# Optimization experiments

Measured on AMD Instinct MI355X. Metric: run time of the kernel, lower is better.

The kernel has to match this reference:

```python
import jax, jax.numpy as jnp
import numpy as np

BN_EPS = 1e-5
NEG_SLOPE = 0.2

def _avgpool2(x):
    B, C, H, W = x.shape
    return x.reshape(B, C, H // 2, 2, W // 2, 2).mean(axis=(3, 5))

def _conv1x1(x, w, b):
    # x: [B,C,H,W], w: [O,C], b: [O]
    return jnp.einsum('bchw,oc->bohw', x, w) + b[None, :, None, None]

def _bilinear_resize(x, out_h, out_w):
    # PyTorch F.interpolate(mode='bilinear', align_corners=False) semantics
    B, C, h, w = x.shape
    ys = jnp.maximum((jnp.arange(out_h, dtype=jnp.float32) + 0.5) * (h / out_h) - 0.5, 0.0)
    xs = jnp.maximum((jnp.arange(out_w, dtype=jnp.float32) + 0.5) * (w / out_w) - 0.5, 0.0)
    y0 = jnp.floor(ys).astype(jnp.int32); x0 = jnp.floor(xs).astype(jnp.int32)
    wy = (ys - y0.astype(jnp.float32)).astype(x.dtype)
    wx = (xs - x0.astype(jnp.float32)).astype(x.dtype)
    y1 = jnp.minimum(y0 + 1, h - 1); x1 = jnp.minimum(x0 + 1, w - 1)
    rows = x[:, :, y0, :] * (1.0 - wy)[None, None, :, None] + x[:, :, y1, :] * wy[None, None, :, None]
    out = rows[:, :, :, x0] * (1.0 - wx)[None, None, None, :] + rows[:, :, :, x1] * wx[None, None, None, :]
    return out

def setup_inputs() -> dict:
    key = jax.random.key(0)
    ks = jax.random.split(key, 16)
    B, Cin, Hid, Cout, H, W = 8, 64, 64, 64, 128, 128
    s = 0.05
    return {
        'rgb': jax.random.normal(ks[0], (B, Cin, H, W), dtype=jnp.float32),
        'freq': jax.random.normal(ks[1], (B, Cin, H, W), dtype=jnp.float32),
        'w_q': jax.random.normal(ks[2], (Hid, Cin), dtype=jnp.float32) * s,
        'b_q': jax.random.normal(ks[3], (Hid,), dtype=jnp.float32) * s,
        'w_k': jax.random.normal(ks[4], (Hid, Cin), dtype=jnp.float32) * s,
        'b_k': jax.random.normal(ks[5], (Hid,), dtype=jnp.float32) * s,
        'w_v': jax.random.normal(ks[6], (Hid, Cin), dtype=jnp.float32) * s,
        'b_v': jax.random.normal(ks[7], (Hid,), dtype=jnp.float32) * s,
        'w_o': jax.random.normal(ks[8], (Cout, Hid), dtype=jnp.float32) * s,
        'b_o': jax.random.normal(ks[9], (Cout,), dtype=jnp.float32) * s,
        'bn_gamma': jnp.ones((Cout,), dtype=jnp.float32),
        'bn_beta': jnp.zeros((Cout,), dtype=jnp.float32),
        'bn_mean': jax.random.normal(ks[10], (Cout,), dtype=jnp.float32) * s,
        'bn_var': jax.random.uniform(ks[11], (Cout,), dtype=jnp.float32, minval=0.5, maxval=1.5),
    }

def reference(rgb, freq, w_q, b_q, w_k, b_k, w_v, b_v, w_o, b_o, bn_gamma, bn_beta, bn_mean, bn_var):
    B, C, H, W = rgb.shape
    rgb_ds = _avgpool2(rgb)
    freq_ds = _avgpool2(freq)
    hd, wd = rgb_ds.shape[2], rgb_ds.shape[3]
    hid = w_q.shape[0]
    scale = hid ** (-0.5)
    # 1x1 conv QKV projections, flatten spatial dims to tokens N = hd*wd
    q = _conv1x1(rgb_ds, w_q, b_q).reshape(B, hid, hd * wd)   # [B,hid,N]
    k = _conv1x1(freq_ds, w_k, b_k).reshape(B, hid, hd * wd)  # [B,hid,N]
    v = _conv1x1(freq_ds, w_v, b_v).reshape(B, hid, hd * wd)  # [B,hid,N]
    attn = jax.nn.softmax(jnp.einsum('bcn,bcm->bnm', q, k) * scale, axis=-1)  # [B,N,N]
    z = jnp.einsum('bnm,bcm->bcn', attn, v).reshape(B, hid, hd, wd)
    z = _bilinear_resize(z, H, W)
    y = _conv1x1(z, w_o, b_o)
    # inference-mode BatchNorm fused as affine
    inv = bn_gamma / jnp.sqrt(bn_var + BN_EPS)
    y = (y - bn_mean[None, :, None, None]) * inv[None, :, None, None] + bn_beta[None, :, None, None]
    y = jnp.where(y >= 0, y, NEG_SLOPE * y)  # LeakyReLU(0.2)
    return rgb + y
```

## Files before the change

kernel.cpp:

```cpp
#include <hip/hip_runtime.h>
#include <hip/hip_bf16.h>

typedef unsigned short u16;
typedef unsigned int   u32;
typedef __attribute__((ext_vector_type(8))) short bf16x8;
typedef __attribute__((ext_vector_type(4))) float f32x4;

__device__ __forceinline__ u16 f2bf(float f) {
  u32 u = __float_as_uint(f);
  u32 r = u + 0x7fffu + ((u >> 16) & 1u);
  return (u16)(r >> 16);
}
__device__ __forceinline__ float bflo(u32 u) { return __uint_as_float(u << 16); }
__device__ __forceinline__ float bfhi(u32 u) { return __uint_as_float(u & 0xffff0000u); }
__device__ __forceinline__ u32 packhi(float a, float b) {
  return __builtin_amdgcn_perm(__float_as_uint(b), __float_as_uint(a), 0x07060302u);
}

__global__ __launch_bounds__(256, 4) void k_qkv(
    const float* __restrict__ rgb, const float* __restrict__ freq,
    const float* __restrict__ wq, const float* __restrict__ bq,
    const float* __restrict__ wk, const float* __restrict__ bk,
    const float* __restrict__ wv, const float* __restrict__ bv,
    u16* __restrict__ Qo, u16* __restrict__ Ko, u16* __restrict__ Vo)
{
  __shared__ __align__(16) u16 sm[3 * 4608];
  u16* X  = sm;
  u16* W0 = sm + 4608;
  u16* W1 = sm + 9216;

  const int t    = threadIdx.x;
  const int side = blockIdx.x & 1;
  const int seg  = blockIdx.x >> 1;
  const int idx0 = seg * 64;
  const int bb   = idx0 >> 12;
  const int n0   = idx0 & 4095;
  const int h    = n0 >> 6;
  const float* src = side ? freq : rgb;

  const size_t sbase = (size_t)bb * 64 * 16384 + (size_t)(2 * h) * 128;
  {
    const int tokp = t & 31;
    const int grp  = t >> 5;
    const float* p0 = src + sbase + 4 * tokp + (size_t)(grp * 8) * 16384;
    u32 pk0[4], pk1[4];
#pragma unroll
    for (int c = 0; c < 8; c += 2) {
      const float* pa = p0 + (size_t)c * 16384;
      float4 a0 = *(const float4*)pa;
      float4 a1 = *(const float4*)(pa + 128);
      float t0a = 0.25f * ((a0.x + a0.y) + (a1.x + a1.y));
      float t1a = 0.25f * ((a0.z + a0.w) + (a1.z + a1.w));
      const float* pb = pa + 16384;
      float4 c0 = *(const float4*)pb;
      float4 c1 = *(const float4*)(pb + 128);
      float t0b = 0.25f * ((c0.x + c0.y) + (c1.x + c1.y));
      float t1b = 0.25f * ((c0.z + c0.w) + (c1.z + c1.w));
      pk0[c >> 1] = (u32)f2bf(t0a) | ((u32)f2bf(t0b) << 16);
      pk1[c >> 1] = (u32)f2bf(t1a) | ((u32)f2bf(t1b) << 16);
    }
    uint4 qv0; qv0.x = pk0[0]; qv0.y = pk0[1]; qv0.z = pk0[2]; qv0.w = pk0[3];
    uint4 qv1; qv1.x = pk1[0]; qv1.y = pk1[1]; qv1.z = pk1[2]; qv1.w = pk1[3];
    *(uint4*)&X[(2 * tokp) * 72 + grp * 8] = qv0;
    *(uint4*)&X[(2 * tokp + 1) * 72 + grp * 8] = qv1;
  }
  {
    const int o = t >> 2, c0 = (t & 3) << 4;
    const float4* p4 = (const float4*)((side ? wk : wq) + o * 64 + c0);
    float4 f0 = p4[0], f1 = p4[1], f2 = p4[2], f3 = p4[3];
    uint4 qa, qb;
    qa.x = (u32)f2bf(f0.x) | ((u32)f2bf(f0.y) << 16);
    qa.y = (u32)f2bf(f0.z) | ((u32)f2bf(f0.w) << 16);
    qa.z = (u32)f2bf(f1.x) | ((u32)f2bf(f1.y) << 16);
    qa.w = (u32)f2bf(f1.z) | ((u32)f2bf(f1.w) << 16);
    qb.x = (u32)f2bf(f2.x) | ((u32)f2bf(f2.y) << 16);
    qb.y = (u32)f2bf(f2.z) | ((u32)f2bf(f2.w) << 16);
    qb.z = (u32)f2bf(f3.x) | ((u32)f2bf(f3.y) << 16);
    qb.w = (u32)f2bf(f3.z) | ((u32)f2bf(f3.w) << 16);
    *(uint4*)&W0[o * 72 + c0] = qa;
    *(uint4*)&W0[o * 72 + c0 + 8] = qb;
    if (side) {
      const float4* v4 = (const float4*)(wv + o * 64 + c0);
      float4 g0 = v4[0], g1 = v4[1], g2 = v4[2], g3 = v4[3];
      qa.x = (u32)f2bf(g0.x) | ((u32)f2bf(g0.y) << 16);
      qa.y = (u32)f2bf(g0.z) | ((u32)f2bf(g0.w) << 16);
      qa.z = (u32)f2bf(g1.x) | ((u32)f2bf(g1.y) << 16);
      qa.w = (u32)f2bf(g1.z) | ((u32)f2bf(g1.w) << 16);
      qb.x = (u32)f2bf(g2.x) | ((u32)f2bf(g2.y) << 16);
      qb.y = (u32)f2bf(g2.z) | ((u32)f2bf(g2.w) << 16);
      qb.z = (u32)f2bf(g3.x) | ((u32)f2bf(g3.y) << 16);
      qb.w = (u32)f2bf(g3.z) | ((u32)f2bf(g3.w) << 16);
      *(uint4*)&W1[o * 72 + c0] = qa;
      *(uint4*)&W1[o * 72 + c0 + 8] = qb;
    }
  }
  __syncthreads();

  const int lane = t & 63, w = t >> 6;
  const int l15 = lane & 15, qd = lane >> 4;
  const int tb = w * 16;

  bf16x8 af0 = *(const bf16x8*)&X[(tb + l15) * 72 + qd * 8];
  bf16x8 af1 = *(const bf16x8*)&X[(tb + l15) * 72 + 32 + qd * 8];

  f32x4 acc[4];
#pragma unroll
  for (int nt = 0; nt < 4; ++nt) {
    bf16x8 b0 = *(const bf16x8*)&W0[(nt * 16 + l15) * 72 + qd * 8];
    bf16x8 b1 = *(const bf16x8*)&W0[(nt * 16 + l15) * 72 + 32 + qd * 8];
    f32x4 a = {0.f, 0.f, 0.f, 0.f};
    a = __builtin_amdgcn_mfma_f32_16x16x32_bf16(af0, b0, a, 0, 0, 0);
    a = __builtin_amdgcn_mfma_f32_16x16x32_bf16(af1, b1, a, 0, 0, 0);
    acc[nt] = a;
  }
  {
    const float* bias0 = side ? bk : bq;
    const float sc = side ? 1.f : 0.18033688f;
    u16* dst0 = side ? Ko : Qo;
#pragma unroll
    for (int nt = 0; nt < 4; ++nt) {
      float bia = bias0[nt * 16 + l15];
#pragma unroll
      for (int e = 0; e < 4; ++e) {
        int tok = idx0 + tb + qd * 4 + e;
        dst0[(size_t)tok * 64 + nt * 16 + l15] = f2bf((acc[nt][e] + bia) * sc);
      }
    }
  }

  if (side) {
    f32x4 accv[4];
#pragma unroll
    for (int ct = 0; ct < 4; ++ct) {
      bf16x8 a0 = *(const bf16x8*)&W1[(ct * 16 + l15) * 72 + qd * 8];
      bf16x8 a1 = *(const bf16x8*)&W1[(ct * 16 + l15) * 72 + 32 + qd * 8];
      f32x4 a = {0.f, 0.f, 0.f, 0.f};
      a = __builtin_amdgcn_mfma_f32_16x16x32_bf16(a0, af0, a, 0, 0, 0);
      a = __builtin_amdgcn_mfma_f32_16x16x32_bf16(a1, af1, a, 0, 0, 0);
      accv[ct] = a;
    }
#pragma unroll
    for (int ct = 0; ct < 4; ++ct) {
#pragma unroll
      for (int e = 0; e < 4; ++e) {
        int c = ct * 16 + qd * 4 + e;
        float v = accv[ct][e] + bv[c];
        Vo[((size_t)(bb * 64 + c)) * 4096 + n0 + tb + l15] = f2bf(v);
      }
    }
  }
}

__global__ __launch_bounds__(256, 2) void k_attn(
    const u16* __restrict__ Qg, const u16* __restrict__ Kg,
    const u16* __restrict__ Vg,
    const float* __restrict__ wo, const float* __restrict__ bo,
    const float* __restrict__ gam, const float* __restrict__ bet,
    const float* __restrict__ mean, const float* __restrict__ var,
    u16* __restrict__ Ya)
{
  __shared__ __align__(16) u16 Pb[4 * 4608];
  __shared__ __align__(16) u16 Wl[4608];
  __shared__ __align__(16) u16 Zc[4608];
  __shared__ float lb[256];
  __shared__ float Afs[64], Bfs[64];

  const int b  = blockIdx.x;
  const int q0 = blockIdx.y * 64;
  const int t  = threadIdx.x;
  const int lane = t & 63, w = t >> 6;
  const int l15 = lane & 15, qd = lane >> 4;
  u16* P = Pb + w * 4608;

  {
    const int o = t >> 2, c0 = (t & 3) << 4;
    const float4* p4 = (const float4*)(wo + o * 64 + c0);
    float4 f0 = p4[0], f1 = p4[1], f2 = p4[2], f3 = p4[3];
    uint4 qa, qb;
    qa.x = (u32)f2bf(f0.x) | ((u32)f2bf(f0.y) << 16);
    qa.y = (u32)f2bf(f0.z) | ((u32)f2bf(f0.w) << 16);
    qa.z = (u32)f2bf(f1.x) | ((u32)f2bf(f1.y) << 16);
    qa.w = (u32)f2bf(f1.z) | ((u32)f2bf(f1.w) << 16);
    qb.x = (u32)f2bf(f2.x) | ((u32)f2bf(f2.y) << 16);
    qb.y = (u32)f2bf(f2.z) | ((u32)f2bf(f2.w) << 16);
    qb.z = (u32)f2bf(f3.x) | ((u32)f2bf(f3.y) << 16);
    qb.w = (u32)f2bf(f3.z) | ((u32)f2bf(f3.w) << 16);
    *(uint4*)&Wl[o * 72 + c0] = qa;
    *(uint4*)&Wl[o * 72 + c0 + 8] = qb;
    if (t < 64) {
      float A = gam[t] * __frsqrt_rn(var[t] + 1e-5f);
      Afs[t] = A;
      Bfs[t] = (bo[t] - mean[t]) * A + bet[t];
    }
  }

  bf16x8 qf[4][2];
#pragma unroll
  for (int qt = 0; qt < 4; ++qt) {
    const u16* p = Qg + ((size_t)(b * 4096 + q0 + qt * 16 + l15)) * 64 + qd * 8;
    qf[qt][0] = *(const bf16x8*)p;
    qf[qt][1] = *(const bf16x8*)(p + 32);
  }

  f32x4 zacc[4][4];
#pragma unroll
  for (int i = 0; i < 4; ++i)
#pragma unroll
    for (int j = 0; j < 4; ++j) {
      f32x4 z = {0.f, 0.f, 0.f, 0.f};
      zacc[i][j] = z;
    }
  float lacc[4] = {0.f, 0.f, 0.f, 0.f};

  for (int tile = 0; tile < 16; ++tile) {
    const int n0 = w * 1024 + tile * 64;

    bf16x8 kf[4][2], vf[4][2];
#pragma unroll
    for (int mt = 0; mt < 4; ++mt) {
      const u16* p = Kg + ((size_t)(b * 4096 + n0 + mt * 16 + l15)) * 64 + qd * 8;
      kf[mt][0] = *(const bf16x8*)p;
      kf[mt][1] = *(const bf16x8*)(p + 32);
    }
#pragma unroll
    for (int ct = 0; ct < 4; ++ct) {
      const u16* p = Vg + ((size_t)(b * 64 + ct * 16 + l15)) * 4096 + n0 + qd * 8;
      vf[ct][0] = *(const bf16x8*)p;
      vf[ct][1] = *(const bf16x8*)(p + 32);
    }

#pragma unroll
    for (int qt = 0; qt < 4; ++qt) {
#pragma unroll
      for (int mt = 0; mt < 4; ++mt) {
        f32x4 a = {0.f, 0.f, 0.f, 0.f};
        __builtin_amdgcn_s_setprio(1);
        a = __builtin_amdgcn_mfma_f32_16x16x32_bf16(kf[mt][0], qf[qt][0], a, 0, 0, 0);
        a = __builtin_amdgcn_mfma_f32_16x16x32_bf16(kf[mt][1], qf[qt][1], a, 0, 0, 0);
        __builtin_amdgcn_s_setprio(0);
        float p0 = __builtin_amdgcn_exp2f(a[0]);
        float p1 = __builtin_amdgcn_exp2f(a[1]);
        float p2 = __builtin_amdgcn_exp2f(a[2]);
        float p3 = __builtin_amdgcn_exp2f(a[3]);
        lacc[qt] += (p0 + p1) + (p2 + p3);
        uint2 pw;
        pw.x = packhi(p0, p1);
        pw.y = packhi(p2, p3);
        *(uint2*)&P[(qt * 16 + l15) * 72 + mt * 16 + qd * 4] = pw;
      }
    }
#pragma unroll
    for (int qt = 0; qt < 4; ++qt) {
      bf16x8 pf0 = *(const bf16x8*)&P[(qt * 16 + l15) * 72 + qd * 8];
      bf16x8 pf1 = *(const bf16x8*)&P[(qt * 16 + l15) * 72 + 32 + qd * 8];
      __builtin_amdgcn_s_setprio(1);
#pragma unroll
      for (int ct = 0; ct < 4; ++ct) {
        zacc[ct][qt] = __builtin_amdgcn_mfma_f32_16x16x32_bf16(vf[ct][0], pf0, zacc[ct][qt], 0, 0, 0);
        zacc[ct][qt] = __builtin_amdgcn_mfma_f32_16x16x32_bf16(vf[ct][1], pf1, zacc[ct][qt], 0, 0, 0);
      }
      __builtin_amdgcn_s_setprio(0);
    }
  }

#pragma unroll
  for (int qt = 0; qt < 4; ++qt) {
    float l = lacc[qt];
    l += __shfl_xor(l, 16);
    l += __shfl_xor(l, 32);
    lb[w * 64 + qt * 16 + l15] = l;
  }
#pragma unroll
  for (int qt = 0; qt < 4; ++qt)
#pragma unroll
    for (int ct = 0; ct < 4; ++ct) {
      uint2 pw;
      pw.x = packhi(zacc[ct][qt][0], zacc[ct][qt][1]);
      pw.y = packhi(zacc[ct][qt][2], zacc[ct][qt][3]);
      *(uint2*)&P[(qt * 16 + l15) * 72 + ct * 16 + qd * 4] = pw;
    }
  __syncthreads();

  {
    const u32* Pu = (const u32*)Pb;
    u32* Zu = (u32*)Zc;
#pragma unroll
    for (int i = 0; i < 8; ++i) {
      int cell = i * 256 + t;
      int q = cell >> 5, cu = cell & 31;
      float s0 = 0.f, s1 = 0.f;
#pragma unroll
      for (int ww = 0; ww < 4; ++ww) {
        u32 v = Pu[ww * 2304 + q * 36 + cu];
        s0 += bflo(v);
        s1 += bfhi(v);
      }
      float inv = 1.f / (lb[q] + lb[64 + q] + lb[128 + q] + lb[192 + q]);
      Zu[q * 36 + cu] = packhi(s0 * inv, s1 * inv);
    }
  }
  __syncthreads();

  {
    u16* Ys = Pb;
    bf16x8 af0 = *(const bf16x8*)&Zc[(w * 16 + l15) * 72 + qd * 8];
    bf16x8 af1 = *(const bf16x8*)&Zc[(w * 16 + l15) * 72 + 32 + qd * 8];
#pragma unroll
    for (int nt = 0; nt < 4; ++nt) {
      bf16x8 b0 = *(const bf16x8*)&Wl[(nt * 16 + l15) * 72 + qd * 8];
      bf16x8 b1 = *(const bf16x8*)&Wl[(nt * 16 + l15) * 72 + 32 + qd * 8];
      f32x4 y = {0.f, 0.f, 0.f, 0.f};
      y = __builtin_amdgcn_mfma_f32_16x16x32_bf16(b0, af0, y, 0, 0, 0);
      y = __builtin_amdgcn_mfma_f32_16x16x32_bf16(b1, af1, y, 0, 0, 0);
#pragma unroll
      for (int e = 0; e < 4; ++e) {
        const int o = nt * 16 + qd * 4 + e;
        float v = y[e] * Afs[o] + Bfs[o];
        Ys[o * 72 + w * 16 + l15] = (u16)(__float_as_uint(v) >> 16);
      }
    }
  }
  __syncthreads();
  {
    const int o = t >> 2, c4 = (t & 3) << 4;
    uint4 y0 = *(const uint4*)&Pb[o * 72 + c4];
    uint4 y1 = *(const uint4*)&Pb[o * 72 + c4 + 8];
    u16* d = Ya + ((size_t)(b * 64 + o)) * 4096 + q0;
    *(uint4*)&d[c4] = y0;
    *(uint4*)&d[c4 + 8] = y1;
  }
}

__global__ __launch_bounds__(256, 8) void k_out(
    const u16* __restrict__ Ya, const float* __restrict__ rgb,
    float* __restrict__ out)
{
  const int tid = blockIdx.x * 256 + threadIdx.x;
  const int g = tid & 31;
  const int i = (tid >> 5) & 127;
  const int o = (tid >> 12) & 63;
  const int b = tid >> 18;

  float ys = fmaxf(0.5f * (float)i - 0.25f, 0.f);
  int   y0 = (int)ys;
  float wy = ys - (float)y0;
  int   y1 = min(y0 + 1, 63);

  const u32* Yw = (const u32*)(Ya + ((size_t)(b * 64 + o)) * 4096);
  const int base0 = y0 * 32, base1 = y1 * 32;
  const int gm = (g == 0) ? 0 : g - 1;
  const int gp = (g == 31) ? 31 : g + 1;

  u32 tm = Yw[base0 + gm], t0 = Yw[base0 + g], tp = Yw[base0 + gp];
  u32 bm = Yw[base1 + gm], b0w = Yw[base1 + g], bp = Yw[base1 + gp];

  const float iw = 1.f - wy;
  float r_m1 = iw * bfhi(tm) + wy * bfhi(bm);
  float r_0  = iw * bflo(t0) + wy * bflo(b0w);
  float r_1  = iw * bfhi(t0) + wy * bfhi(b0w);
  float r_2  = iw * bflo(tp) + wy * bflo(bp);

  float v0 = (g == 0)  ? r_0 : 0.25f * r_m1 + 0.75f * r_0;
  float v1 = 0.75f * r_0 + 0.25f * r_1;
  float v2 = 0.25f * r_0 + 0.75f * r_1;
  float v3 = (g == 31) ? r_1 : 0.75f * r_1 + 0.25f * r_2;

  v0 = (v0 >= 0.f) ? v0 : 0.2f * v0;
  v1 = (v1 >= 0.f) ? v1 : 0.2f * v1;
  v2 = (v2 >= 0.f) ? v2 : 0.2f * v2;
  v3 = (v3 >= 0.f) ? v3 : 0.2f * v3;

  const size_t pix = ((size_t)((b * 64 + o) * 128 + i)) * 128 + g * 4;
  float4 rv = *(const float4*)(rgb + pix);
  float4 ov;
  ov.x = rv.x + v0;
  ov.y = rv.y + v1;
  ov.z = rv.z + v2;
  ov.w = rv.w + v3;
  *(float4*)(out + pix) = ov;
}

extern "C" void kernel_launch(void* const* d_in, const int* in_sizes, int n_in,
                              void* d_out, int out_size, void* d_ws, size_t ws_size,
                              hipStream_t stream) {
  (void)in_sizes; (void)n_in; (void)out_size; (void)ws_size;
  const float* rgb  = (const float*)d_in[0];
  const float* freq = (const float*)d_in[1];
  const float* wq   = (const float*)d_in[2];
  const float* bq   = (const float*)d_in[3];
  const float* wk   = (const float*)d_in[4];
  const float* bk   = (const float*)d_in[5];
  const float* wv   = (const float*)d_in[6];
  const float* bv   = (const float*)d_in[7];
  const float* wo   = (const float*)d_in[8];
  const float* bo   = (const float*)d_in[9];
  const float* gam  = (const float*)d_in[10];
  const float* bet  = (const float*)d_in[11];
  const float* mean = (const float*)d_in[12];
  const float* var  = (const float*)d_in[13];

  char* ws = (char*)d_ws;
  u16* Qw = (u16*)(ws);
  u16* Kw = (u16*)(ws + 4194304);
  u16* Vw = (u16*)(ws + 8388608);
  u16* Yw = (u16*)(ws + 12582912);

  k_qkv<<<dim3(1024), dim3(256), 0, stream>>>(rgb, freq, wq, bq, wk, bk, wv, bv,
                                              Qw, Kw, Vw);
  k_attn<<<dim3(8, 64), dim3(256), 0, stream>>>(Qw, Kw, Vw, wo, bo, gam, bet,
                                                mean, var, Yw);
  k_out<<<dim3(8192), dim3(256), 0, stream>>>(Yw, rgb, (float*)d_out);
}
```

Measured before the change: 200.7 us.

## Halve attention query tile per block and split keys across two wave pairs

The attention kernel now handles 32 queries per block instead of 64, launching twice as many blocks. Waves are arranged as 2 query halves × 2 key splits instead of 4 key splits, with per-wave register and shared-memory footprints shrunk and launch bounds raised for higher occupancy. This targets low occupancy and poor latency hiding from large per-wave accumulators, at the cost of reloading each K/V tile for half as many queries, which doubles K/V global traffic.

Result: slower. 361.0 us (+79.9%).

```diff
diff --git a/kernel.cpp b/kernel.cpp
--- a/kernel.cpp
+++ b/kernel.cpp
@@ -151,7 +151,7 @@
   }
 }
 
-__global__ __launch_bounds__(256, 2) void k_attn(
+__global__ __launch_bounds__(256, 4) void k_attn(
     const u16* __restrict__ Qg, const u16* __restrict__ Kg,
     const u16* __restrict__ Vg,
     const float* __restrict__ wo, const float* __restrict__ bo,
@@ -159,18 +159,19 @@
     const float* __restrict__ mean, const float* __restrict__ var,
     u16* __restrict__ Ya)
 {
-  __shared__ __align__(16) u16 Pb[4 * 4608];
+  __shared__ __align__(16) u16 Pb[4 * 1152];
   __shared__ __align__(16) u16 Wl[4608];
-  __shared__ __align__(16) u16 Zc[4608];
-  __shared__ float lb[256];
+  __shared__ __align__(16) u16 Zc[2304];
+  __shared__ float lb[64];
   __shared__ float Afs[64], Bfs[64];
 
   const int b  = blockIdx.x;
-  const int q0 = blockIdx.y * 64;
+  const int q0 = blockIdx.y * 32;
   const int t  = threadIdx.x;
   const int lane = t & 63, w = t >> 6;
+  const int qh = w & 1, ks = w >> 1;
   const int l15 = lane & 15, qd = lane >> 4;
-  u16* P = Pb + w * 4608;
+  u16* P = Pb + w * 1152;
 
   {
     const int o = t >> 2, c0 = (t & 3) << 4;
@@ -194,34 +195,51 @@
     }
   }
 
-  bf16x8 qf[4][2];
-#pragma unroll
-  for (int qt = 0; qt < 4; ++qt) {
-    const u16* p = Qg + ((size_t)(b * 4096 + q0 + qt * 16 + l15)) * 64 + qd * 8;
-    qf[qt][0] = *(const bf16x8*)p;
-    qf[qt][1] = *(const bf16x8*)(p + 32);
-  }
-
-  f32x4 zacc[4][4];
-#pragma unroll
-  for (int i = 0; i < 4; ++i)
-#pragma unroll
-    for (int j = 0; j < 4; ++j) {
-      f32x4 z = {0.f, 0.f, 0.f, 0.f};
-      zacc[i][j] = z;
-    }
-  float lacc[4] = {0.f, 0.f, 0.f, 0.f};
-
-  for (int tile = 0; tile < 16; ++tile) {
-    const int n0 = w * 1024 + tile * 64;
-
-    bf16x8 kf[4][2], vf[4][2];
+  bf16x8 qf0, qf1;
+  {
+    const u16* p = Qg + ((size_t)(b * 4096 + q0 + qh * 16 + l15)) * 64 + qd * 8;
+    qf0 = *(const bf16x8*)p;
+    qf1 = *(const bf16x8*)(p + 32);
+  }
+
+  f32x4 zacc[4];
+#pragma unroll
+  for (int i = 0; i < 4; ++i) {
+    f32x4 z = {0.f, 0.f, 0.f, 0.f};
+    zacc[i] = z;
+  }
+  float lacc = 0.f;
+
+  for (int tile = 0; tile < 32; ++tile) {
+    const int n0 = ks * 2048 + tile * 64;
+
+    bf16x8 kf[4][2];
 #pragma unroll
     for (int mt = 0; mt < 4; ++mt) {
       const u16* p = Kg + ((size_t)(b * 4096 + n0 + mt * 16 + l15)) * 64 + qd * 8;
       kf[mt][0] = *(const bf16x8*)p;
       kf[mt][1] = *(const bf16x8*)(p + 32);
     }
+
+#pragma unroll
+    for (int mt = 0; mt < 4; ++mt) {
+      f32x4 a = {0.f, 0.f, 0.f, 0.f};
+      __builtin_amdgcn_s_setprio(1);
+      a = __builtin_amdgcn_mfma_f32_16x16x32_bf16(kf[mt][0], qf0, a, 0, 0, 0);
+      a = __builtin_amdgcn_mfma_f32_16x16x32_bf16(kf[mt][1], qf1, a, 0, 0, 0);
+      __builtin_amdgcn_s_setprio(0);
+      float p0 = __builtin_amdgcn_exp2f(a[0]);
+      float p1 = __builtin_amdgcn_exp2f(a[1]);
+      float p2 = __builtin_amdgcn_exp2f(a[2]);
+      float p3 = __builtin_amdgcn_exp2f(a[3]);
+      lacc += (p0 + p1) + (p2 + p3);
+      uint2 pw;
+      pw.x = packhi(p0, p1);
+      pw.y = packhi(p2, p3);
+      *(uint2*)&P[l15 * 72 + mt * 16 + qd * 4] = pw;
+    }
+
+    bf16x8 vf[4][2];
 #pragma unroll
     for (int ct = 0; ct < 4; ++ct) {
       const u16* p = Vg + ((size_t)(b * 64 + ct * 16 + l15)) * 4096 + n0 + qd * 8;
@@ -229,73 +247,47 @@
       vf[ct][1] = *(const bf16x8*)(p + 32);
     }
 
-#pragma unroll
-    for (int qt = 0; qt < 4; ++qt) {
-#pragma unroll
-      for (int mt = 0; mt < 4; ++mt) {
-        f32x4 a = {0.f, 0.f, 0.f, 0.f};
-        __builtin_amdgcn_s_setprio(1);
-        a = __builtin_amdgcn_mfma_f32_16x16x32_bf16(kf[mt][0], qf[qt][0], a, 0, 0, 0);
-        a = __builtin_amdgcn_mfma_f32_16x16x32_bf16(kf[mt][1], qf[qt][1], a, 0, 0, 0);
-        __builtin_amdgcn_s_setprio(0);
-        float p0 = __builtin_amdgcn_exp2f(a[0]);
-        float p1 = __builtin_amdgcn_exp2f(a[1]);
-        float p2 = __builtin_amdgcn_exp2f(a[2]);
-        float p3 = __builtin_amdgcn_exp2f(a[3]);
-        lacc[qt] += (p0 + p1) + (p2 + p3);
-        uint2 pw;
-        pw.x = packhi(p0, p1);
-        pw.y = packhi(p2, p3);
-        *(uint2*)&P[(qt * 16 + l15) * 72 + mt * 16 + qd * 4] = pw;
-      }
-    }
-#pragma unroll
-    for (int qt = 0; qt < 4; ++qt) {
-      bf16x8 pf0 = *(const bf16x8*)&P[(qt * 16 + l15) * 72 + qd * 8];
-      bf16x8 pf1 = *(const bf16x8*)&P[(qt * 16 + l15) * 72 + 32 + qd * 8];
+    {
+      bf16x8 pf0 = *(const bf16x8*)&P[l15 * 72 + qd * 8];
+      bf16x8 pf1 = *(const bf16x8*)&P[l15 * 72 + 32 + qd * 8];
       __builtin_amdgcn_s_setprio(1);
 #pragma unroll
       for (int ct = 0; ct < 4; ++ct) {
-        zacc[ct][qt] = __builtin_amdgcn_mfma_f32_16x16x32_bf16(vf[ct][0], pf0, zacc[ct][qt], 0, 0, 0);
-        zacc[ct][qt] = __builtin_amdgcn_mfma_f32_16x16x32_bf16(vf[ct][1], pf1, zacc[ct][qt], 0, 0, 0);
+        zacc[ct] = __builtin_amdgcn_mfma_f32_16x16x32_bf16(vf[ct][0], pf0, zacc[ct], 0, 0, 0);
+        zacc[ct] = __builtin_amdgcn_mfma_f32_16x16x32_bf16(vf[ct][1], pf1, zacc[ct], 0, 0, 0);
       }
       __builtin_amdgcn_s_setprio(0);
     }
   }
 
-#pragma unroll
-  for (int qt = 0; qt < 4; ++qt) {
-    float l = lacc[qt];
+  {
+    float l = lacc;
     l += __shfl_xor(l, 16);
     l += __shfl_xor(l, 32);
-    lb[w * 64 + qt * 16 + l15] = l;
-  }
-#pragma unroll
-  for (int qt = 0; qt < 4; ++qt)
-#pragma unroll
-    for (int ct = 0; ct < 4; ++ct) {
-      uint2 pw;
-      pw.x = packhi(zacc[ct][qt][0], zacc[ct][qt][1]);
-      pw.y = packhi(zacc[ct][qt][2], zacc[ct][qt][3]);
-      *(uint2*)&P[(qt * 16 + l15) * 72 + ct * 16 + qd * 4] = pw;
-    }
+    lb[w * 16 + l15] = l;
+  }
+#pragma unroll
+  for (int ct = 0; ct < 4; ++ct) {
+    uint2 pw;
+    pw.x = packhi(zacc[ct][0], zacc[ct][1]);
+    pw.y = packhi(zacc[ct][2], zacc[ct][3]);
+    *(uint2*)&P[l15 * 72 + ct * 16 + qd * 4] = pw;
+  }
   __syncthreads();
 
   {
     const u32* Pu = (const u32*)Pb;
     u32* Zu = (u32*)Zc;
 #pragma unroll
-    for (int i = 0; i < 8; ++i) {
+    for (int i = 0; i < 4; ++i) {
       int cell = i * 256 + t;
       int q = cell >> 5, cu = cell & 31;
-      float s0 = 0.f, s1 = 0.f;
-#pragma unroll
-      for (int ww = 0; ww < 4; ++ww) {
-        u32 v = Pu[ww * 2304 + q * 36 + cu];
-        s0 += bflo(v);
-        s1 += bfhi(v);
-      }
-      float inv = 1.f / (lb[q] + lb[64 + q] + lb[128 + q] + lb[192 + q]);
+      int qh2 = q >> 4, qq = q & 15;
+      u32 v0 = Pu[(qh2) * 576 + qq * 36 + cu];
+      u32 v1 = Pu[(2 + qh2) * 576 + qq * 36 + cu];
+      float s0 = bflo(v0) + bflo(v1);
+      float s1 = bfhi(v0) + bfhi(v1);
+      float inv = 1.f / (lb[qh2 * 16 + qq] + lb[(2 + qh2) * 16 + qq]);
       Zu[q * 36 + cu] = packhi(s0 * inv, s1 * inv);
     }
   }
@@ -303,31 +295,29 @@
 
   {
     u16* Ys = Pb;
-    bf16x8 af0 = *(const bf16x8*)&Zc[(w * 16 + l15) * 72 + qd * 8];
-    bf16x8 af1 = *(const bf16x8*)&Zc[(w * 16 + l15) * 72 + 32 + qd * 8];
-#pragma unroll
-    for (int nt = 0; nt < 4; ++nt) {
-      bf16x8 b0 = *(const bf16x8*)&Wl[(nt * 16 + l15) * 72 + qd * 8];
-      bf16x8 b1 = *(const bf16x8*)&Wl[(nt * 16 + l15) * 72 + 32 + qd * 8];
+    bf16x8 b0 = *(const bf16x8*)&Wl[(w * 16 + l15) * 72 + qd * 8];
+    bf16x8 b1 = *(const bf16x8*)&Wl[(w * 16 + l15) * 72 + 32 + qd * 8];
+#pragma unroll
+    for (int qt2 = 0; qt2 < 2; ++qt2) {
+      bf16x8 af0 = *(const bf16x8*)&Zc[(qt2 * 16 + l15) * 72 + qd * 8];
+      bf16x8 af1 = *(const bf16x8*)&Zc[(qt2 * 16 + l15) * 72 + 32 + qd * 8];
       f32x4 y = {0.f, 0.f, 0.f, 0.f};
       y = __builtin_amdgcn_mfma_f32_16x16x32_bf16(b0, af0, y, 0, 0, 0);
       y = __builtin_amdgcn_mfma_f32_16x16x32_bf16(b1, af1, y, 0, 0, 0);
 #pragma unroll
       for (int e = 0; e < 4; ++e) {
-        const int o = nt * 16 + qd * 4 + e;
+        const int o = w * 16 + qd * 4 + e;
         float v = y[e] * Afs[o] + Bfs[o];
-        Ys[o * 72 + w * 16 + l15] = (u16)(__float_as_uint(v) >> 16);
+        Ys[o * 40 + qt2 * 16 + l15] = (u16)(__float_as_uint(v) >> 16);
       }
     }
   }
   __syncthreads();
   {
-    const int o = t >> 2, c4 = (t & 3) << 4;
-    uint4 y0 = *(const uint4*)&Pb[o * 72 + c4];
-    uint4 y1 = *(const uint4*)&Pb[o * 72 + c4 + 8];
+    const int o = t >> 2, c4 = (t & 3) << 3;
+    uint4 y0 = *(const uint4*)&Pb[o * 40 + c4];
     u16* d = Ya + ((size_t)(b * 64 + o)) * 4096 + q0;
     *(uint4*)&d[c4] = y0;
-    *(uint4*)&d[c4 + 8] = y1;
   }
 }
 
@@ -407,7 +397,7 @@
 
   k_qkv<<<dim3(1024), dim3(256), 0, stream>>>(rgb, freq, wq, bq, wk, bk, wv, bv,
                                               Qw, Kw, Vw);
-  k_attn<<<dim3(8, 64), dim3(256), 0, stream>>>(Qw, Kw, Vw, wo, bo, gam, bet,
-                                                mean, var, Yw);
+  k_attn<<<dim3(8, 128), dim3(256), 0, stream>>>(Qw, Kw, Vw, wo, bo, gam, bet,
+                                                 mean, var, Yw);
   k_out<<<dim3(8192), dim3(256), 0, stream>>>(Yw, rgb, (float*)d_out);
 }
```
